# Performance work log

Hardware: AMD Instinct MI355X
Metric: run time of the kernel (lower is better)

Reference implementation:

```python
import jax, jax.numpy as jnp
import numpy as np

B, C = 1048576, 40
ALPHA = 0.5          # additive offset so distance factor is never 0
NORMALISE = 1.0      # opt['hier_normalise']


def setup_inputs() -> dict:
    key = jax.random.key(0)
    k1, k2, k3 = jax.random.split(key, 3)
    logits = jax.random.normal(k1, (B, C), dtype=jnp.float32)
    labels = jax.random.randint(k2, (B,), 0, C, dtype=jnp.int32)
    dis_matrix = jax.random.uniform(k3, (C, C), dtype=jnp.float32)
    return {"logits": logits, "labels": labels, "dis_matrix": dis_matrix}


def reference(logits, labels, dis_matrix):
    # per-sample cross entropy (reduction='none')
    logp = jax.nn.log_softmax(logits, axis=-1)                      # [B, C]
    ce = -jnp.take_along_axis(logp, labels[:, None].astype(jnp.int32), axis=-1)[:, 0]  # [B]
    # argmax predictions (done on host in the original; pure gather here)
    pred = jnp.argmax(logits, axis=-1)                              # [B]
    # distance_factor = DIS_MATRIX[gold, pred] + alpha   (non-LCA path)
    distance_factor = dis_matrix[labels, pred] + ALPHA              # [B]
    total_loss = jnp.mean(ce * distance_factor) / NORMALISE
    return total_loss, distance_factor
```

## Files before the change

### kernel.cpp

```cpp
#include <hip/hip_runtime.h>
#include <hip/hip_bf16.h>


#define HDL_B 1048576
#define HDL_C 40
#define HDL_ALPHA 0.5f
#define HDL_BLOCK 256
#define HDL_ROWS 256
#define HDL_GRID (HDL_B / HDL_ROWS)
#define HDL_HALF 128
#define HDL_PAD 41

__global__ __launch_bounds__(HDL_BLOCK)
void hdl_main(const float* __restrict__ logits,
              const int* __restrict__ labels,
              const float* __restrict__ dis,
              float* __restrict__ out,
              float* __restrict__ bsum) {
    __shared__ float tile[HDL_HALF * HDL_PAD];
    __shared__ float wpart[HDL_BLOCK / 64];

    const int tid = threadIdx.x;
    const int row = blockIdx.x * HDL_ROWS + tid;

    const int lab = labels[row];

    const float4* gsrc = reinterpret_cast<const float4*>(logits)
                         + (size_t)blockIdx.x * (HDL_ROWS * HDL_C / 4);

    float x[HDL_C];
    float xl = 0.0f;
    const int myhalf = tid >> 7;
    const int lr_mine = tid & (HDL_HALF - 1);

#pragma unroll
    for (int p = 0; p < 2; ++p) {
#pragma unroll
        for (int k = 0; k < 5; ++k) {
            const int q = tid + HDL_BLOCK * k;
            float4 v = gsrc[p * (HDL_HALF * HDL_C / 4) + q];
            const int lr = q / 10;
            const int c4 = q - lr * 10;
            const int off = lr * HDL_PAD + c4 * 4;
            tile[off + 0] = v.x;
            tile[off + 1] = v.y;
            tile[off + 2] = v.z;
            tile[off + 3] = v.w;
        }
        __syncthreads();
        if (myhalf == p) {
            const int base = lr_mine * HDL_PAD;
#pragma unroll
            for (int j = 0; j < HDL_C; ++j)
                x[j] = tile[base + j];
            xl = tile[base + lab];
        }
        __syncthreads();
    }

    float m = x[0];
    int pred = 0;
#pragma unroll
    for (int j = 1; j < HDL_C; ++j) {
        const bool g = x[j] > m;
        m = g ? x[j] : m;
        pred = g ? j : pred;
    }

    const float L2E = 1.4426950408889634f;
    const float mL = m * L2E;
    float s = 0.0f;
#pragma unroll
    for (int j = 0; j < HDL_C; ++j)
        s += __builtin_amdgcn_exp2f(__builtin_fmaf(x[j], L2E, -mL));

    const float ce = (m - xl) + 0.69314718055994531f * __builtin_amdgcn_logf(s);

    const float df = dis[lab * HDL_C + pred] + HDL_ALPHA;
    out[1 + row] = df;

    float val = ce * df;

#pragma unroll
    for (int o = 32; o > 0; o >>= 1)
        val += __shfl_down(val, o, 64);
    const int lane = tid & 63;
    const int wid = tid >> 6;
    if (lane == 0) wpart[wid] = val;
    __syncthreads();
    if (tid == 0)
        bsum[blockIdx.x] = wpart[0] + wpart[1] + wpart[2] + wpart[3];
}

__global__ __launch_bounds__(256)
void hdl_finalize(const float* __restrict__ bsum,
                  float* __restrict__ out) {
    __shared__ double dpart[4];
    const int tid = threadIdx.x;
    double v = 0.0;
#pragma unroll
    for (int k = 0; k < HDL_GRID / 256; ++k)
        v += (double)bsum[tid + 256 * k];
#pragma unroll
    for (int o = 32; o > 0; o >>= 1)
        v += __shfl_down(v, o, 64);
    if ((tid & 63) == 0) dpart[tid >> 6] = v;
    __syncthreads();
    if (tid == 0) {
        const double tot = dpart[0] + dpart[1] + dpart[2] + dpart[3];
        out[0] = (float)(tot * (1.0 / (double)HDL_B));
    }
}

extern "C" void kernel_launch(void* const* d_in, const int* in_sizes, int n_in,
                              void* d_out, int out_size, void* d_ws, size_t ws_size,
                              hipStream_t stream) {
    const float* logits = (const float*)d_in[0];
    const int*   labels = (const int*)d_in[1];
    const float* dis    = (const float*)d_in[2];
    float* out  = (float*)d_out;
    float* bsum = (float*)d_ws;

    hdl_main<<<HDL_GRID, HDL_BLOCK, 0, stream>>>(logits, labels, dis, out, bsum);
    hdl_finalize<<<1, 256, 0, stream>>>(bsum, out);
}
```

Before: 237.7 us.

## Issue all global loads upfront and transpose LDS tile to column-major

```diff
diff --git a/kernel.cpp b/kernel.cpp
--- a/kernel.cpp
+++ b/kernel.cpp
@@ -9,53 +9,73 @@
 #define HDL_ROWS 256
 #define HDL_GRID (HDL_B / HDL_ROWS)
 #define HDL_HALF 128
-#define HDL_PAD 41
+#define HDL_CSTR (HDL_HALF + 1)
 
-__global__ __launch_bounds__(HDL_BLOCK)
+__global__ __launch_bounds__(HDL_BLOCK, 5)
 void hdl_main(const float* __restrict__ logits,
               const int* __restrict__ labels,
               const float* __restrict__ dis,
               float* __restrict__ out,
               float* __restrict__ bsum) {
-    __shared__ float tile[HDL_HALF * HDL_PAD];
+    __shared__ float tile[HDL_C * HDL_CSTR];
     __shared__ float wpart[HDL_BLOCK / 64];
 
     const int tid = threadIdx.x;
     const int row = blockIdx.x * HDL_ROWS + tid;
-
     const int lab = labels[row];
 
     const float4* gsrc = reinterpret_cast<const float4*>(logits)
                          + (size_t)blockIdx.x * (HDL_ROWS * HDL_C / 4);
 
+    float4 v[5], w[5];
+#pragma unroll
+    for (int k = 0; k < 5; ++k)
+        v[k] = gsrc[tid + HDL_BLOCK * k];
+#pragma unroll
+    for (int k = 0; k < 5; ++k)
+        w[k] = gsrc[HDL_HALF * HDL_C / 4 + tid + HDL_BLOCK * k];
+
     float x[HDL_C];
     float xl = 0.0f;
-    const int myhalf = tid >> 7;
     const int lr_mine = tid & (HDL_HALF - 1);
 
 #pragma unroll
-    for (int p = 0; p < 2; ++p) {
+    for (int k = 0; k < 5; ++k) {
+        const int q = tid + HDL_BLOCK * k;
+        const int lr = q / 10;
+        const int c4 = q - lr * 10;
+        const int cb = 4 * c4;
+        tile[(cb + 0) * HDL_CSTR + lr] = v[k].x;
+        tile[(cb + 1) * HDL_CSTR + lr] = v[k].y;
+        tile[(cb + 2) * HDL_CSTR + lr] = v[k].z;
+        tile[(cb + 3) * HDL_CSTR + lr] = v[k].w;
+    }
+    __syncthreads();
+    if (tid < HDL_HALF) {
 #pragma unroll
-        for (int k = 0; k < 5; ++k) {
-            const int q = tid + HDL_BLOCK * k;
-            float4 v = gsrc[p * (HDL_HALF * HDL_C / 4) + q];
-            const int lr = q / 10;
-            const int c4 = q - lr * 10;
-            const int off = lr * HDL_PAD + c4 * 4;
-            tile[off + 0] = v.x;
-            tile[off + 1] = v.y;
-            tile[off + 2] = v.z;
-            tile[off + 3] = v.w;
-        }
-        __syncthreads();
-        if (myhalf == p) {
-            const int base = lr_mine * HDL_PAD;
+        for (int j = 0; j < HDL_C; ++j)
+            x[j] = tile[j * HDL_CSTR + lr_mine];
+        xl = tile[lab * HDL_CSTR + lr_mine];
+    }
+    __syncthreads();
+
 #pragma unroll
-            for (int j = 0; j < HDL_C; ++j)
-                x[j] = tile[base + j];
-            xl = tile[base + lab];
-        }
-        __syncthreads();
+    for (int k = 0; k < 5; ++k) {
+        const int q = tid + HDL_BLOCK * k;
+        const int lr = q / 10;
+        const int c4 = q - lr * 10;
+        const int cb = 4 * c4;
+        tile[(cb + 0) * HDL_CSTR + lr] = w[k].x;
+        tile[(cb + 1) * HDL_CSTR + lr] = w[k].y;
+        tile[(cb + 2) * HDL_CSTR + lr] = w[k].z;
+        tile[(cb + 3) * HDL_CSTR + lr] = w[k].w;
+    }
+    __syncthreads();
+    if (tid >= HDL_HALF) {
+#pragma unroll
+        for (int j = 0; j < HDL_C; ++j)
+            x[j] = tile[j * HDL_CSTR + lr_mine];
+        xl = tile[lab * HDL_CSTR + lr_mine];
     }
 
     float m = x[0];
```

Result: no change. 237.4 us, median of 2 (-0.1%).
